# Kernel tuning notes

Hardware: AMD Instinct MI355X
Metric: run time of the kernel (lower is better)

## Reference

```python
import jax, jax.numpy as jnp
import numpy as np

N, IN_DIM, OUT_DIM = 8192, 128, 128

def setup_inputs() -> dict:
    key = jax.random.key(0)
    k1, k2, k3, k4 = jax.random.split(key, 4)
    X = jax.random.normal(k1, (N, IN_DIM), dtype=jnp.float32)
    A = jax.random.uniform(k2, (N, N), dtype=jnp.float32)
    # nn.Linear(in_dim, out_dim): W [out,in], b [out]
    bound = 1.0 / np.sqrt(IN_DIM)
    W = jax.random.uniform(k3, (OUT_DIM, IN_DIM), minval=-bound, maxval=bound, dtype=jnp.float32)
    b = jax.random.uniform(k4, (OUT_DIM,), minval=-bound, maxval=bound, dtype=jnp.float32)
    return {"X": X, "A": A, "W": W, "b": b}

def reference(X, A, W, b):
    n = A.shape[0]
    A_hat = A + jnp.eye(n, dtype=A.dtype)                 # A + I
    d_inv_sqrt = A_hat.sum(axis=1) ** -0.5                # [N]
    # D^-1/2 @ A_hat @ D^-1/2 == row/col scaling (same math, no diag GEMMs)
    A_norm = d_inv_sqrt[:, None] * A_hat * d_inv_sqrt[None, :]
    H = A_norm @ X                                        # [N, in_dim]
    return H @ W.T + b                                    # [N, out_dim]
```

## Files before the change

### kernel.cpp

```cpp
#include <hip/hip_runtime.h>

#define N_NODES 8192
#define DIM 128

typedef short bf16x8 __attribute__((ext_vector_type(8)));
typedef float f32x4 __attribute__((ext_vector_type(4)));

__device__ __forceinline__ unsigned short f2bf_rne(float x) {
    unsigned int u = __builtin_bit_cast(unsigned int, x);
    u += 0x7fffu + ((u >> 16) & 1u);
    return (unsigned short)(u >> 16);
}
__device__ __forceinline__ float bf2f(unsigned short h) {
    unsigned int u = ((unsigned int)h) << 16;
    return __builtin_bit_cast(float, u);
}

__global__ __launch_bounds__(256) void k_rowsum(const float* __restrict__ A,
                                                float* __restrict__ d) {
    int row = blockIdx.x;
    const float4* Ar = (const float4*)(A + (size_t)row * N_NODES);
    int t = threadIdx.x;
    float s = 0.f;
#pragma unroll
    for (int i = 0; i < 8; ++i) {
        float4 v = Ar[t + i * 256];
        s += (v.x + v.y) + (v.z + v.w);
    }
#pragma unroll
    for (int off = 32; off > 0; off >>= 1)
        s += __shfl_down(s, off, 64);
    __shared__ float wsum[4];
    if ((t & 63) == 0) wsum[t >> 6] = s;
    __syncthreads();
    if (t == 0) {
        float tot = wsum[0] + wsum[1] + wsum[2] + wsum[3] + 1.0f;
        d[row] = rsqrtf(tot);
    }
}

__global__ __launch_bounds__(256) void k_zgemm(const float* __restrict__ X,
                                               const float* __restrict__ W,
                                               const float* __restrict__ d,
                                               unsigned short* __restrict__ Zt) {
    __shared__ float Xs[64][129];
    __shared__ float Ws[64][129];
    int rb = blockIdx.x >> 1;
    int cb = blockIdx.x & 1;
    int t = threadIdx.x;
    const float4* Xg = (const float4*)(X + (size_t)rb * 64 * DIM);
    const float4* Wg = (const float4*)(W + (size_t)cb * 64 * DIM);
#pragma unroll
    for (int i = 0; i < 8; ++i) {
        int f = t + i * 256;
        int r = f >> 5;
        int c = (f & 31) << 2;
        float4 v = Xg[f];
        Xs[r][c] = v.x; Xs[r][c + 1] = v.y; Xs[r][c + 2] = v.z; Xs[r][c + 3] = v.w;
        float4 w = Wg[f];
        Ws[r][c] = w.x; Ws[r][c + 1] = w.y; Ws[r][c + 2] = w.z; Ws[r][c + 3] = w.w;
    }
    __syncthreads();
    int tx = t & 15, ty = t >> 4;
    float acc[4][4] = {};
    for (int k = 0; k < DIM; ++k) {
        float xr[4], wr[4];
#pragma unroll
        for (int i = 0; i < 4; ++i) xr[i] = Xs[ty * 4 + i][k];
#pragma unroll
        for (int j = 0; j < 4; ++j) wr[j] = Ws[tx * 4 + j][k];
#pragma unroll
        for (int i = 0; i < 4; ++i)
#pragma unroll
            for (int j = 0; j < 4; ++j)
                acc[i][j] += xr[i] * wr[j];
    }
#pragma unroll
    for (int i = 0; i < 4; ++i) {
        int row = rb * 64 + ty * 4 + i;
        float dv = d[row];
#pragma unroll
        for (int j = 0; j < 4; ++j) {
            int col = cb * 64 + tx * 4 + j;
            Zt[(size_t)col * N_NODES + row] = f2bf_rne(dv * acc[i][j]);
        }
    }
}

__global__ __launch_bounds__(64) void k_spmm(const float* __restrict__ A,
                                             const unsigned short* __restrict__ Zt,
                                             const float* __restrict__ d,
                                             const float* __restrict__ bias,
                                             float* __restrict__ out) {
    int lane = threadIdx.x;
    int l15 = lane & 15, quad = lane >> 4;
    int row0 = blockIdx.x * 16;

    const float* Arow = A + (size_t)(row0 + l15) * N_NODES + quad * 8;
    const unsigned short* Zb = Zt + (size_t)l15 * N_NODES + quad * 8;

    f32x4 acc[8];
#pragma unroll
    for (int i = 0; i < 8; ++i) acc[i] = (f32x4){0.f, 0.f, 0.f, 0.f};

    for (int k = 0; k < N_NODES; k += 32) {
        f32x4 a0 = *(const f32x4*)(Arow + k);
        f32x4 a1 = *((const f32x4*)(Arow + k) + 1);
        bf16x8 af;
        af[0] = (short)f2bf_rne(a0[0]); af[1] = (short)f2bf_rne(a0[1]);
        af[2] = (short)f2bf_rne(a0[2]); af[3] = (short)f2bf_rne(a0[3]);
        af[4] = (short)f2bf_rne(a1[0]); af[5] = (short)f2bf_rne(a1[1]);
        af[6] = (short)f2bf_rne(a1[2]); af[7] = (short)f2bf_rne(a1[3]);
        bf16x8 bfr[8];
#pragma unroll
        for (int n = 0; n < 8; ++n)
            bfr[n] = *(const bf16x8*)(Zb + (size_t)n * 16 * N_NODES + k);
#pragma unroll
        for (int n = 0; n < 8; ++n)
            acc[n] = __builtin_amdgcn_mfma_f32_16x16x32_bf16(af, bfr[n], acc[n], 0, 0, 0);
    }

#pragma unroll
    for (int n = 0; n < 8; ++n) {
        int col = n * 16 + l15;
        float bcol = bias[col];
#pragma unroll
        for (int r = 0; r < 4; ++r) {
            int row = row0 + quad * 4 + r;
            float zid = bf2f(Zt[(size_t)col * N_NODES + row]);
            out[(size_t)row * DIM + col] = d[row] * (acc[n][r] + zid) + bcol;
        }
    }
}

extern "C" void kernel_launch(void* const* d_in, const int* in_sizes, int n_in,
                              void* d_out, int out_size, void* d_ws, size_t ws_size,
                              hipStream_t stream) {
    const float* X = (const float*)d_in[0];
    const float* A = (const float*)d_in[1];
    const float* W = (const float*)d_in[2];
    const float* b = (const float*)d_in[3];
    float* out = (float*)d_out;

    char* ws = (char*)d_ws;
    float* dinv = (float*)ws;
    unsigned short* Zt = (unsigned short*)(ws + 32768);

    k_rowsum<<<N_NODES, 256, 0, stream>>>(A, dinv);
    k_zgemm<<<256, 256, 0, stream>>>(X, W, dinv, Zt);
    k_spmm<<<512, 64, 0, stream>>>(A, Zt, dinv, b, out);
}
```

Before: 521.6 us.

## Stage A tiles in swizzled LDS with double buffering across four waves

The spmm kernel moves from one wave per 16-row block to four waves that each own 32 output columns. The 16-row A tile is loaded with coalesced reads, converted to bf16 once, and stored in XOR-swizzled shared memory. The next 512-column chunk is prefetched into registers while MFMAs run on the current chunk. This cuts redundant per-lane conversions, improves A access coalescing and overlaps global loads with compute. In exchange it adds LDS traffic, a barrier per chunk and higher register pressure.

```diff
diff --git a/kernel.cpp b/kernel.cpp
--- a/kernel.cpp
+++ b/kernel.cpp
@@ -4,6 +4,7 @@
 #define DIM 128
 
 typedef short bf16x8 __attribute__((ext_vector_type(8)));
+typedef unsigned short u16x4 __attribute__((ext_vector_type(4)));
 typedef float f32x4 __attribute__((ext_vector_type(4)));
 
 __device__ __forceinline__ unsigned short f2bf_rne(float x) {
@@ -87,48 +88,91 @@
     }
 }
 
-__global__ __launch_bounds__(64) void k_spmm(const float* __restrict__ A,
-                                             const unsigned short* __restrict__ Zt,
-                                             const float* __restrict__ d,
-                                             const float* __restrict__ bias,
-                                             float* __restrict__ out) {
-    int lane = threadIdx.x;
-    int l15 = lane & 15, quad = lane >> 4;
-    int row0 = blockIdx.x * 16;
+__global__ __launch_bounds__(256) void k_spmm(const float* __restrict__ A,
+                                              const unsigned short* __restrict__ Zt,
+                                              const float* __restrict__ d,
+                                              const float* __restrict__ bias,
+                                              float* __restrict__ out) {
+    __shared__ unsigned short As[2][16 * 512];
+    const int t = threadIdx.x;
+    const int lane = t & 63;
+    const int wv = t >> 6;
+    const int l15 = lane & 15, quad = lane >> 4;
+    const int row0 = blockIdx.x * 16;
 
-    const float* Arow = A + (size_t)(row0 + l15) * N_NODES + quad * 8;
-    const unsigned short* Zb = Zt + (size_t)l15 * N_NODES + quad * 8;
+    const int colb = wv * 32;
+    const unsigned short* Zb = Zt + (size_t)(colb + l15) * N_NODES + quad * 8;
 
-    f32x4 acc[8];
+    f32x4 acc0 = {0.f, 0.f, 0.f, 0.f}, acc1 = {0.f, 0.f, 0.f, 0.f};
+
+    const float* Ag0 = A + (size_t)row0 * N_NODES;
+
 #pragma unroll
-    for (int i = 0; i < 8; ++i) acc[i] = (f32x4){0.f, 0.f, 0.f, 0.f};
+    for (int i = 0; i < 8; ++i) {
+        int flat = t + i * 256;
+        int r = flat >> 7;
+        int c4 = (flat & 127) << 2;
+        f32x4 v = *(const f32x4*)(Ag0 + (size_t)r * N_NODES + c4);
+        int byte = (r * 1024 + c4 * 2) ^ ((r & 7) << 4);
+        u16x4 pk = { f2bf_rne(v[0]), f2bf_rne(v[1]), f2bf_rne(v[2]), f2bf_rne(v[3]) };
+        *(u16x4*)((char*)As[0] + byte) = pk;
+    }
+    __syncthreads();
 
-    for (int k = 0; k < N_NODES; k += 32) {
-        f32x4 a0 = *(const f32x4*)(Arow + k);
-        f32x4 a1 = *((const f32x4*)(Arow + k) + 1);
-        bf16x8 af;
-        af[0] = (short)f2bf_rne(a0[0]); af[1] = (short)f2bf_rne(a0[1]);
-        af[2] = (short)f2bf_rne(a0[2]); af[3] = (short)f2bf_rne(a0[3]);
-        af[4] = (short)f2bf_rne(a1[0]); af[5] = (short)f2bf_rne(a1[1]);
-        af[6] = (short)f2bf_rne(a1[2]); af[7] = (short)f2bf_rne(a1[3]);
-        bf16x8 bfr[8];
+    int cur = 0;
+    for (int chunk = 0; chunk < 16; ++chunk) {
+        const int kbase = chunk * 512;
+
+        f32x4 pre0, pre1, pre2, pre3, pre4, pre5, pre6, pre7;
+        if (chunk < 15) {
+            const float* Ag = Ag0 + kbase + 512;
+#define LDPRE(ii, dst)                                                   \
+            {   int flat = t + (ii) * 256;                               \
+                int r = flat >> 7; int c4 = (flat & 127) << 2;           \
+                dst = *(const f32x4*)(Ag + (size_t)r * N_NODES + c4); }
+            LDPRE(0, pre0) LDPRE(1, pre1) LDPRE(2, pre2) LDPRE(3, pre3)
+            LDPRE(4, pre4) LDPRE(5, pre5) LDPRE(6, pre6) LDPRE(7, pre7)
+#undef LDPRE
+        }
+
+        const char* Ab = (const char*)As[cur];
 #pragma unroll
-        for (int n = 0; n < 8; ++n)
-            bfr[n] = *(const bf16x8*)(Zb + (size_t)n * 16 * N_NODES + k);
-#pragma unroll
-        for (int n = 0; n < 8; ++n)
-            acc[n] = __builtin_amdgcn_mfma_f32_16x16x32_bf16(af, bfr[n], acc[n], 0, 0, 0);
+        for (int ks = 0; ks < 16; ++ks) {
+            int abyte = (l15 * 1024 + (ks * 32 + quad * 8) * 2) ^ ((l15 & 7) << 4);
+            bf16x8 af = *(const bf16x8*)(Ab + abyte);
+            bf16x8 b0 = *(const bf16x8*)(Zb + kbase + ks * 32);
+            bf16x8 b1 = *(const bf16x8*)(Zb + (size_t)16 * N_NODES + kbase + ks * 32);
+            acc0 = __builtin_amdgcn_mfma_f32_16x16x32_bf16(af, b0, acc0, 0, 0, 0);
+            acc1 = __builtin_amdgcn_mfma_f32_16x16x32_bf16(af, b1, acc1, 0, 0, 0);
+        }
+
+        if (chunk < 15) {
+            unsigned short* Ao = (unsigned short*)As[cur ^ 1];
+#define STPRE(ii, src)                                                   \
+            {   int flat = t + (ii) * 256;                               \
+                int r = flat >> 7; int c4 = (flat & 127) << 2;           \
+                int byte = (r * 1024 + c4 * 2) ^ ((r & 7) << 4);         \
+                u16x4 pk = { f2bf_rne(src[0]), f2bf_rne(src[1]),         \
+                             f2bf_rne(src[2]), f2bf_rne(src[3]) };       \
+                *(u16x4*)((char*)Ao + byte) = pk; }
+            STPRE(0, pre0) STPRE(1, pre1) STPRE(2, pre2) STPRE(3, pre3)
+            STPRE(4, pre4) STPRE(5, pre5) STPRE(6, pre6) STPRE(7, pre7)
+#undef STPRE
+            __syncthreads();
+            cur ^= 1;
+        }
     }
 
 #pragma unroll
-    for (int n = 0; n < 8; ++n) {
-        int col = n * 16 + l15;
+    for (int n = 0; n < 2; ++n) {
+        int col = colb + n * 16 + l15;
         float bcol = bias[col];
+        f32x4 a = n ? acc1 : acc0;
 #pragma unroll
         for (int r = 0; r < 4; ++r) {
             int row = row0 + quad * 4 + r;
             float zid = bf2f(Zt[(size_t)col * N_NODES + row]);
-            out[(size_t)row * DIM + col] = d[row] * (acc[n][r] + zid) + bcol;
+            out[(size_t)row * DIM + col] = d[row] * (a[r] + zid) + bcol;
         }
     }
 }
@@ -148,5 +192,5 @@
 
     k_rowsum<<<N_NODES, 256, 0, stream>>>(A, dinv);
     k_zgemm<<<256, 256, 0, stream>>>(X, W, dinv, Zt);
-    k_spmm<<<512, 64, 0, stream>>>(A, Zt, dinv, b, out);
+    k_spmm<<<512, 256, 0, stream>>>(A, Zt, dinv, b, out);
 }
```

Result: no change. 511.4 us (-1.9%).

## Pre-pack A into bf16 MFMA fragments during rowsum and split-K the aggregation

Applied to the files above, without the earlier changes.

The row-sum pass now also converts A to bf16 and writes it in an MFMA-fragment-ready layout through a swizzled LDS tile. The aggregation GEMM then reads half the bytes of A, and its loads are contiguous per lane. Z is likewise stored pre-packed in fragment order. The aggregation kernel moves to 512-thread blocks that split K across 8 waves and reduce through shared memory, raising parallelism per row block. The cost is an extra 128MB bf16 write and read of A and a shared-memory reduction.

```diff
diff --git a/kernel.cpp b/kernel.cpp
--- a/kernel.cpp
+++ b/kernel.cpp
@@ -4,6 +4,7 @@
 #define DIM 128
 
 typedef short bf16x8 __attribute__((ext_vector_type(8)));
+typedef unsigned short u16x4 __attribute__((ext_vector_type(4)));
 typedef float f32x4 __attribute__((ext_vector_type(4)));
 
 __device__ __forceinline__ unsigned short f2bf_rne(float x) {
@@ -16,33 +17,71 @@
     return __builtin_bit_cast(float, u);
 }
 
-__global__ __launch_bounds__(256) void k_rowsum(const float* __restrict__ A,
-                                                float* __restrict__ d) {
-    int row = blockIdx.x;
-    const float4* Ar = (const float4*)(A + (size_t)row * N_NODES);
-    int t = threadIdx.x;
-    float s = 0.f;
-#pragma unroll
-    for (int i = 0; i < 8; ++i) {
-        float4 v = Ar[t + i * 256];
-        s += (v.x + v.y) + (v.z + v.w);
-    }
-#pragma unroll
-    for (int off = 32; off > 0; off >>= 1)
-        s += __shfl_down(s, off, 64);
-    __shared__ float wsum[4];
-    if ((t & 63) == 0) wsum[t >> 6] = s;
+__global__ __launch_bounds__(256) void k_prep(const float* __restrict__ A,
+                                              unsigned short* __restrict__ Abp,
+                                              float* __restrict__ d) {
+    __shared__ unsigned short tile[16 * 512];
+    __shared__ float rs[2][8][128];
+    const int t = threadIdx.x;
+    const int lane = t & 63, wv = t >> 6;
+    const int l15 = lane & 15, quad = lane >> 4;
+    const int rb16 = blockIdx.x;
+    const float* Ag0 = A + (size_t)rb16 * 16 * N_NODES;
+    const int h = t >> 7;
+    const int c4 = (t & 127) << 2;
+    float rsum[8] = {};
+
+    f32x4 pre[8];
+#pragma unroll
+    for (int i = 0; i < 8; ++i)
+        pre[i] = *(const f32x4*)(Ag0 + (size_t)(h + 2 * i) * N_NODES + c4);
+
+    for (int chunk = 0; chunk < 16; ++chunk) {
+        f32x4 curv[8];
+#pragma unroll
+        for (int i = 0; i < 8; ++i) curv[i] = pre[i];
+        if (chunk < 15) {
+            const float* Ag = Ag0 + (chunk + 1) * 512;
+#pragma unroll
+            for (int i = 0; i < 8; ++i)
+                pre[i] = *(const f32x4*)(Ag + (size_t)(h + 2 * i) * N_NODES + c4);
+        }
+        __syncthreads();
+#pragma unroll
+        for (int i = 0; i < 8; ++i) {
+            int r = h + 2 * i;
+            f32x4 v = curv[i];
+            rsum[i] += (v[0] + v[1]) + (v[2] + v[3]);
+            int byte = (r * 1024 + c4 * 2) ^ ((r & 7) << 4);
+            u16x4 pk = { f2bf_rne(v[0]), f2bf_rne(v[1]), f2bf_rne(v[2]), f2bf_rne(v[3]) };
+            *(u16x4*)((char*)tile + byte) = pk;
+        }
+        __syncthreads();
+#pragma unroll
+        for (int u = 0; u < 4; ++u) {
+            int kk = wv * 4 + u;
+            int abyte = (l15 * 1024 + (kk * 32 + quad * 8) * 2) ^ ((l15 & 7) << 4);
+            bf16x8 frag = *(const bf16x8*)((const char*)tile + abyte);
+            int kbg = chunk * 16 + kk;
+            *(bf16x8*)(Abp + ((size_t)(rb16 * 256 + kbg) * 64 + lane) * 8) = frag;
+        }
+    }
+
+#pragma unroll
+    for (int i = 0; i < 8; ++i) rs[h][i][t & 127] = rsum[i];
     __syncthreads();
-    if (t == 0) {
-        float tot = wsum[0] + wsum[1] + wsum[2] + wsum[3] + 1.0f;
-        d[row] = rsqrtf(tot);
+    if (t < 16) {
+        const float* p = rs[t & 1][t >> 1];
+        float s = 0.f;
+        for (int j = 0; j < 128; ++j) s += p[j];
+        d[rb16 * 16 + t] = rsqrtf(s + 1.0f);
     }
 }
 
 __global__ __launch_bounds__(256) void k_zgemm(const float* __restrict__ X,
                                                const float* __restrict__ W,
                                                const float* __restrict__ d,
-                                               unsigned short* __restrict__ Zt) {
+                                               unsigned short* __restrict__ Zp) {
     __shared__ float Xs[64][129];
     __shared__ float Ws[64][129];
     int rb = blockIdx.x >> 1;
@@ -79,56 +118,69 @@
     for (int i = 0; i < 4; ++i) {
         int row = rb * 64 + ty * 4 + i;
         float dv = d[row];
+        int kb = row >> 5, jj = row & 7;
+        int lrow = ((row >> 3) & 3) * 16;
 #pragma unroll
         for (int j = 0; j < 4; ++j) {
             int col = cb * 64 + tx * 4 + j;
-            Zt[(size_t)col * N_NODES + row] = f2bf_rne(dv * acc[i][j]);
-        }
-    }
-}
-
-__global__ __launch_bounds__(64) void k_spmm(const float* __restrict__ A,
-                                             const unsigned short* __restrict__ Zt,
-                                             const float* __restrict__ d,
-                                             const float* __restrict__ bias,
-                                             float* __restrict__ out) {
-    int lane = threadIdx.x;
-    int l15 = lane & 15, quad = lane >> 4;
-    int row0 = blockIdx.x * 16;
-
-    const float* Arow = A + (size_t)(row0 + l15) * N_NODES + quad * 8;
-    const unsigned short* Zb = Zt + (size_t)l15 * N_NODES + quad * 8;
+            int lanep = lrow + (col & 15);
+            Zp[((size_t)(kb * 8 + (col >> 4)) * 64 + lanep) * 8 + jj] =
+                f2bf_rne(dv * acc[i][j]);
+        }
+    }
+}
+
+__global__ __launch_bounds__(512, 4) void k_spmm(const unsigned short* __restrict__ Abp,
+                                                 const unsigned short* __restrict__ Zp,
+                                                 const float* __restrict__ d,
+                                                 const float* __restrict__ bias,
+                                                 float* __restrict__ out) {
+    const int t = threadIdx.x;
+    const int lane = t & 63, wv = t >> 6;
+    const int l15 = lane & 15, quad = lane >> 4;
+    const int rb16 = blockIdx.x;
+    const int row0 = rb16 * 16;
+
+    const unsigned short* Ab = Abp + ((size_t)rb16 * 256 * 64 + lane) * 8;
+    const unsigned short* Zb = Zp + (size_t)lane * 8;
 
     f32x4 acc[8];
 #pragma unroll
-    for (int i = 0; i < 8; ++i) acc[i] = (f32x4){0.f, 0.f, 0.f, 0.f};
-
-    for (int k = 0; k < N_NODES; k += 32) {
-        f32x4 a0 = *(const f32x4*)(Arow + k);
-        f32x4 a1 = *((const f32x4*)(Arow + k) + 1);
-        bf16x8 af;
-        af[0] = (short)f2bf_rne(a0[0]); af[1] = (short)f2bf_rne(a0[1]);
-        af[2] = (short)f2bf_rne(a0[2]); af[3] = (short)f2bf_rne(a0[3]);
-        af[4] = (short)f2bf_rne(a1[0]); af[5] = (short)f2bf_rne(a1[1]);
-        af[6] = (short)f2bf_rne(a1[2]); af[7] = (short)f2bf_rne(a1[3]);
-        bf16x8 bfr[8];
-#pragma unroll
-        for (int n = 0; n < 8; ++n)
-            bfr[n] = *(const bf16x8*)(Zb + (size_t)n * 16 * N_NODES + k);
-#pragma unroll
-        for (int n = 0; n < 8; ++n)
-            acc[n] = __builtin_amdgcn_mfma_f32_16x16x32_bf16(af, bfr[n], acc[n], 0, 0, 0);
-    }
-
-#pragma unroll
-    for (int n = 0; n < 8; ++n) {
-        int col = n * 16 + l15;
+    for (int c = 0; c < 8; ++c) acc[c] = (f32x4){0.f, 0.f, 0.f, 0.f};
+
+#pragma unroll 2
+    for (int kb = wv * 32; kb < wv * 32 + 32; ++kb) {
+        bf16x8 af = *(const bf16x8*)(Ab + (size_t)kb * 512);
+        const unsigned short* zk = Zb + (size_t)kb * 4096;
+#pragma unroll
+        for (int c = 0; c < 8; ++c) {
+            bf16x8 b = *(const bf16x8*)(zk + c * 512);
+            acc[c] = __builtin_amdgcn_mfma_f32_16x16x32_bf16(af, b, acc[c], 0, 0, 0);
+        }
+    }
+
+    __shared__ float red[8][64][33];
+#pragma unroll
+    for (int c = 0; c < 8; ++c)
+#pragma unroll
+        for (int r = 0; r < 4; ++r)
+            red[wv][lane][c * 4 + r] = acc[c][r];
+    __syncthreads();
+
+    {
+        int col = wv * 16 + l15;
         float bcol = bias[col];
 #pragma unroll
         for (int r = 0; r < 4; ++r) {
+            int idx = wv * 4 + r;
+            float s = 0.f;
+#pragma unroll
+            for (int w = 0; w < 8; ++w) s += red[w][lane][idx];
             int row = row0 + quad * 4 + r;
-            float zid = bf2f(Zt[(size_t)col * N_NODES + row]);
-            out[(size_t)row * DIM + col] = d[row] * (acc[n][r] + zid) + bcol;
+            int kb = row >> 5, jj = row & 7;
+            int lanep = ((row >> 3) & 3) * 16 + l15;
+            float zid = bf2f(Zp[((size_t)(kb * 8 + wv) * 64 + lanep) * 8 + jj]);
+            out[(size_t)row * DIM + col] = d[row] * (s + zid) + bcol;
         }
     }
 }
@@ -144,9 +196,10 @@
 
     char* ws = (char*)d_ws;
     float* dinv = (float*)ws;
-    unsigned short* Zt = (unsigned short*)(ws + 32768);
-
-    k_rowsum<<<N_NODES, 256, 0, stream>>>(A, dinv);
-    k_zgemm<<<256, 256, 0, stream>>>(X, W, dinv, Zt);
-    k_spmm<<<512, 64, 0, stream>>>(A, Zt, dinv, b, out);
-}
+    unsigned short* Zp = (unsigned short*)(ws + 32768);
+    unsigned short* Abp = (unsigned short*)(ws + 32768 + (2u << 20));
+
+    k_prep<<<512, 256, 0, stream>>>(A, Abp, dinv);
+    k_zgemm<<<256, 256, 0, stream>>>(X, W, dinv, Zp);
+    k_spmm<<<512, 512, 0, stream>>>(Abp, Zp, dinv, b, out);
+}
```

After: 451.7 us. 13.4% less time.
